# Optimization experiments

Hardware: AMD Instinct MI355X
Metric: run time of the kernel (lower is better)

The kernel has to match this reference:

```python
import jax, jax.numpy as jnp
import numpy as np
import math

T_LEN, BATCH, DIN, DH, DT = 512, 64, 512, 512, 128


def _u(key, shape, std):
    return jax.random.uniform(key, shape, jnp.float32, -std, std)


def setup_inputs() -> dict:
    key = jax.random.key(0)
    ks = jax.random.split(key, 32)
    std = 1.0 / math.sqrt(DH)
    inp = {
        'x': jax.random.normal(ks[0], (T_LEN, BATCH, DIN), jnp.float32),
        'topic': jax.random.normal(ks[1], (BATCH, DT), jnp.float32),
        'mask': jnp.ones((T_LEN, BATCH), jnp.float32),
        # weights stored as [in, out] (transpose of nn.Linear), uniform(-std, std)
        'W_x2zr': _u(ks[2], (DIN, 2 * DH), std),
        'W_tp2zr_x': _u(ks[3], (DT, 2 * DH), std),
        'W_xtp2z': _u(ks[4], (DH, DH), std),
        'b_xtp2z': _u(ks[5], (DH,), std),
        'W_xtp2r': _u(ks[6], (DH, DH), std),
        'b_xtp2r': _u(ks[7], (DH,), std),
        'W_h2zr': _u(ks[8], (DH, 2 * DH), std),
        'W_tp2zr_h': _u(ks[9], (DT, 2 * DH), std),
        'W_htp2z': _u(ks[10], (DH, DH), std),
        'W_htp2r': _u(ks[11], (DH, DH), std),
        'W_x2h': _u(ks[12], (DIN, DH), std),
        'W_tp2h_x': _u(ks[13], (DT, DH), std),
        'W_xtp2h': _u(ks[14], (DH, DH), std),
        'b_xtp2h': _u(ks[15], (DH,), std),
        'W_h2h': _u(ks[16], (DH, DH), std),
        'W_tp2h_h': _u(ks[17], (DT, DH), std),
        'W_htp2h': _u(ks[18], (DH, DH), std),
    }
    return inp


def _tpgru_forward(x, topic, mask,
                   W_x2zr, W_tp2zr_x, W_xtp2z, b_xtp2z, W_xtp2r, b_xtp2r,
                   W_h2zr, W_tp2zr_h, W_htp2z, W_htp2r,
                   W_x2h, W_tp2h_x, W_xtp2h, b_xtp2h,
                   W_h2h, W_tp2h_h, W_htp2h):
    # Precompute all time-parallel (input-side) projections outside the scan.
    ZR_x = x @ W_x2zr                          # [T,B,2H]
    tp_zr_x = topic @ W_tp2zr_x                # [B,2H]
    tp_zr_h = topic @ W_tp2zr_h                # [B,2H]
    Z_xtp, R_xtp = jnp.split(ZR_x * tp_zr_x[None], 2, axis=-1)
    ZR_xtp = jnp.concatenate([Z_xtp @ W_xtp2z + b_xtp2z,
                              R_xtp @ W_xtp2r + b_xtp2r], axis=-1)  # [T,B,2H]
    tp_h_x = topic @ W_tp2h_x                  # [B,H]
    tp_h_h = topic @ W_tp2h_h                  # [B,H]
    H_xtp = ((x @ W_x2h) * tp_h_x[None]) @ W_xtp2h + b_xtp2h        # [T,B,H]

    def step(h_, inputs):
        zr_xtp, h_xtp, m = inputs              # [B,2H], [B,H], [B]
        zr_htp = (h_ @ W_h2zr) * tp_zr_h
        z_htp, r_htp = jnp.split(zr_htp, 2, axis=-1)
        pre_zr = jax.nn.sigmoid(zr_xtp + jnp.concatenate(
            [z_htp @ W_htp2z, r_htp @ W_htp2r], axis=-1))
        z, r = jnp.split(pre_zr, 2, axis=-1)
        h = jnp.tanh(h_xtp + r * (((h_ @ W_h2h) * tp_h_h) @ W_htp2h))
        h = (1.0 - z) * h + z * h_
        m = m[:, None]
        h = m * h + (1.0 - m) * h_
        return h, h

    h0 = jnp.zeros((x.shape[1], W_h2h.shape[0]), x.dtype)
    hT, output = jax.lax.scan(step, h0, (ZR_xtp, H_xtp, mask))
    return output, hT[None]                    # [T,B,H], [1,B,H]


def reference(x, topic, mask,
              W_x2zr, W_tp2zr_x, W_xtp2z, b_xtp2z, W_xtp2r, b_xtp2r,
              W_h2zr, W_tp2zr_h, W_htp2z, W_htp2r,
              W_x2h, W_tp2h_x, W_xtp2h, b_xtp2h,
              W_h2h, W_tp2h_h, W_htp2h):
    return _tpgru_forward(x, topic, mask,
                          W_x2zr, W_tp2zr_x, W_xtp2z, b_xtp2z, W_xtp2r, b_xtp2r,
                          W_h2zr, W_tp2zr_h, W_htp2z, W_htp2r,
                          W_x2h, W_tp2h_x, W_xtp2h, b_xtp2h,
                          W_h2h, W_tp2h_h, W_htp2h)
```

## Files before the change

### kernel.cpp

```cpp
#include <hip/hip_runtime.h>
#include <stdint.h>
#include <stddef.h>


#define T_LEN 512
#define BATCH 64
#define DIN   512
#define DH    512
#define DT    128

typedef __attribute__((ext_vector_type(8))) short short8;
typedef __attribute__((ext_vector_type(4))) float f32x4;

static __device__ __forceinline__ float bf2f(unsigned short u) {
  unsigned v = ((unsigned)u) << 16;
  return __builtin_bit_cast(float, v);
}
static __device__ __forceinline__ unsigned short f2bf(float f) {
  unsigned v = __builtin_bit_cast(unsigned, f);
  unsigned r = (v + 0x7fffu + ((v >> 16) & 1u)) >> 16;
  return (unsigned short)r;
}
static __device__ __forceinline__ float sigmoid_f(float x) {
  return 1.f / (1.f + __expf(-x));
}
static __device__ __forceinline__ float tanh_f(float x) {
  float e = __expf(-2.f * fabsf(x));
  float t = (1.f - e) / (1.f + e);
  return copysignf(t, x);
}

__global__ __launch_bounds__(256) void k_cvt(const float* __restrict__ src,
                                             unsigned short* __restrict__ dst,
                                             int n8) {
  for (int idx = blockIdx.x * 256 + threadIdx.x; idx < n8; idx += gridDim.x * 256) {
    const float4* s = (const float4*)src + 2 * (size_t)idx;
    float4 a = s[0], b = s[1];
    unsigned short d[8];
    d[0] = f2bf(a.x); d[1] = f2bf(a.y); d[2] = f2bf(a.z); d[3] = f2bf(a.w);
    d[4] = f2bf(b.x); d[5] = f2bf(b.y); d[6] = f2bf(b.z); d[7] = f2bf(b.w);
    *(uint4*)(dst + (size_t)idx * 8) = *(const uint4*)d;
  }
}

__global__ __launch_bounds__(256) void k_tr(const float* __restrict__ src,
                                            unsigned short* __restrict__ dst,
                                            int K, int N) {
  __shared__ float t[32][33];
  const int tx = threadIdx.x & 31, ty = threadIdx.x >> 5;
  const int k0 = blockIdx.y * 32, n0 = blockIdx.x * 32;
  for (int i = ty; i < 32; i += 8)
    t[i][tx] = src[(size_t)(k0 + i) * N + n0 + tx];
  __syncthreads();
  for (int i = ty; i < 32; i += 8)
    dst[(size_t)(n0 + i) * K + k0 + tx] = f2bf(t[tx][i]);
}

__global__ __launch_bounds__(256) void k_topic(
    const float* __restrict__ topic,
    const float* __restrict__ Wzx,
    const float* __restrict__ Wzh,
    const float* __restrict__ Whx,
    const float* __restrict__ Whh,
    float* __restrict__ tzx, float* __restrict__ tzh,
    float* __restrict__ thx, float* __restrict__ thh)
{
  const int b = blockIdx.x;
  __shared__ float tp[DT];
  if (threadIdx.x < DT) tp[threadIdx.x] = topic[b * DT + threadIdx.x];
  __syncthreads();
  for (int c = threadIdx.x; c < 3072; c += 256) {
    const float* wp; float* op; int ld, cc;
    if (c < 1024)      { wp = Wzx; ld = 1024; cc = c;        op = &tzx[b*1024 + cc]; }
    else if (c < 2048) { wp = Wzh; ld = 1024; cc = c - 1024; op = &tzh[b*1024 + cc]; }
    else if (c < 2560) { wp = Whx; ld = 512;  cc = c - 2048; op = &thx[b*512  + cc]; }
    else               { wp = Whh; ld = 512;  cc = c - 2560; op = &thh[b*512  + cc]; }
    float acc = 0.f;
    #pragma unroll 4
    for (int k = 0; k < DT; ++k) acc += tp[k] * wp[(size_t)k * ld + cc];
    *op = acc;
  }
}

template<int EPI>
__global__ __launch_bounds__(256) void gemm128(
    const unsigned short* __restrict__ A, int lda,
    const unsigned short* __restrict__ BT, int ldb,
    const float* __restrict__ rs, int ldrs,
    const float* __restrict__ bias,
    unsigned short* __restrict__ C, int ldc, int K)
{
  __shared__ unsigned short As[128][48];
  __shared__ unsigned short Bs[128][48];
  const int tid = threadIdx.x;
  const int n0 = blockIdx.x * 128;
  const int m0 = blockIdx.y * 128;
  const int wv = tid >> 6, lane = tid & 63;
  const int lh = lane & 15, quad = lane >> 4, q8 = quad * 8;
  const int wr = wv >> 1, wc = wv & 1;
  const int srow = tid >> 1, scol = (tid & 1) * 16;

  f32x4 acc[4][4] = {};

  for (int k0 = 0; k0 < K; k0 += 32) {
    uint4 a4[2], b4[2];
    {
      const unsigned short* ap = A  + (size_t)(m0 + srow) * lda + k0 + scol;
      const unsigned short* bp = BT + (size_t)(n0 + srow) * ldb + k0 + scol;
      a4[0] = ((const uint4*)ap)[0]; a4[1] = ((const uint4*)ap)[1];
      b4[0] = ((const uint4*)bp)[0]; b4[1] = ((const uint4*)bp)[1];
    }
    __syncthreads();
    *(uint4*)(&As[srow][scol])     = a4[0];
    *(uint4*)(&As[srow][scol + 8]) = a4[1];
    *(uint4*)(&Bs[srow][scol])     = b4[0];
    *(uint4*)(&Bs[srow][scol + 8]) = b4[1];
    __syncthreads();
    short8 af[4], bf[4];
    #pragma unroll
    for (int i = 0; i < 4; ++i) {
      af[i] = *(const short8*)(&As[wr * 64 + i * 16 + lh][q8]);
      bf[i] = *(const short8*)(&Bs[wc * 64 + i * 16 + lh][q8]);
    }
    #pragma unroll
    for (int i = 0; i < 4; ++i)
      #pragma unroll
      for (int j = 0; j < 4; ++j)
        acc[i][j] = __builtin_amdgcn_mfma_f32_16x16x32_bf16(af[i], bf[j], acc[i][j], 0, 0, 0);
  }

  #pragma unroll
  for (int i = 0; i < 4; ++i)
    #pragma unroll
    for (int j = 0; j < 4; ++j)
      #pragma unroll
      for (int r = 0; r < 4; ++r) {
        int row = m0 + wr * 64 + i * 16 + quad * 4 + r;
        int col = n0 + wc * 64 + j * 16 + lh;
        float v = acc[i][j][r];
        if (EPI == 0) v *= rs[(size_t)(row & 63) * ldrs + col];
        else          v += bias[col];
        C[(size_t)row * ldc + col] = f2bf(v);
      }
}

__global__ __launch_bounds__(256) void k_comb128(
    const float* __restrict__ W1, int ld1, int off1,
    const unsigned short* __restrict__ W2T,
    const float* __restrict__ S, int ldS, int offS,
    unsigned short* __restrict__ Cout)
{
  __shared__ unsigned short As[128][48];
  __shared__ unsigned short Bs[128][48];
  __shared__ float sS[512];
  const int tid = threadIdx.x;
  const int n0 = blockIdx.x * 128;
  const int m0 = blockIdx.y * 128;
  const int b  = blockIdx.z;
  const int wv = tid >> 6, lane = tid & 63;
  const int lh = lane & 15, quad = lane >> 4, q8 = quad * 8;
  const int wr = wv >> 1, wc = wv & 1;
  const int srow = tid >> 1, scol = (tid & 1) * 16;

  sS[tid]       = S[(size_t)b * ldS + offS + tid];
  sS[tid + 256] = S[(size_t)b * ldS + offS + tid + 256];
  __syncthreads();

  f32x4 acc[4][4] = {};

  for (int k0 = 0; k0 < 512; k0 += 32) {
    unsigned short a8[16]; uint4 b4[2];
    {
      const float* ap = W1 + (size_t)(m0 + srow) * ld1 + off1 + k0 + scol;
      const unsigned short* bp = W2T + (size_t)(n0 + srow) * 512 + k0 + scol;
      b4[0] = ((const uint4*)bp)[0]; b4[1] = ((const uint4*)bp)[1];
      float4 f0 = ((const float4*)ap)[0], f1 = ((const float4*)ap)[1];
      float4 f2 = ((const float4*)ap)[2], f3 = ((const float4*)ap)[3];
      const float* sp = &sS[k0 + scol];
      a8[0]  = f2bf(f0.x * sp[0]);  a8[1]  = f2bf(f0.y * sp[1]);
      a8[2]  = f2bf(f0.z * sp[2]);  a8[3]  = f2bf(f0.w * sp[3]);
      a8[4]  = f2bf(f1.x * sp[4]);  a8[5]  = f2bf(f1.y * sp[5]);
      a8[6]  = f2bf(f1.z * sp[6]);  a8[7]  = f2bf(f1.w * sp[7]);
      a8[8]  = f2bf(f2.x * sp[8]);  a8[9]  = f2bf(f2.y * sp[9]);
      a8[10] = f2bf(f2.z * sp[10]); a8[11] = f2bf(f2.w * sp[11]);
      a8[12] = f2bf(f3.x * sp[12]); a8[13] = f2bf(f3.y * sp[13]);
      a8[14] = f2bf(f3.z * sp[14]); a8[15] = f2bf(f3.w * sp[15]);
    }
    __syncthreads();
    *(uint4*)(&As[srow][scol])     = *(const uint4*)(a8);
    *(uint4*)(&As[srow][scol + 8]) = *(const uint4*)(a8 + 8);
    *(uint4*)(&Bs[srow][scol])     = b4[0];
    *(uint4*)(&Bs[srow][scol + 8]) = b4[1];
    __syncthreads();
    short8 af[4], bf[4];
    #pragma unroll
    for (int i = 0; i < 4; ++i) {
      af[i] = *(const short8*)(&As[wr * 64 + i * 16 + lh][q8]);
      bf[i] = *(const short8*)(&Bs[wc * 64 + i * 16 + lh][q8]);
    }
    #pragma unroll
    for (int i = 0; i < 4; ++i)
      #pragma unroll
      for (int j = 0; j < 4; ++j)
        acc[i][j] = __builtin_amdgcn_mfma_f32_16x16x32_bf16(af[i], bf[j], acc[i][j], 0, 0, 0);
  }

  #pragma unroll
  for (int i = 0; i < 4; ++i)
    #pragma unroll
    for (int j = 0; j < 4; ++j)
      #pragma unroll
      for (int r = 0; r < 4; ++r) {
        int row = m0 + wr * 64 + i * 16 + quad * 4 + r;
        int col = n0 + wc * 64 + j * 16 + lh;
        Cout[(size_t)b * 262144 + (size_t)row * 512 + col] = f2bf(acc[i][j][r]);
      }
}

__global__ __launch_bounds__(512) void k_quant(
    const unsigned short* __restrict__ tmp,
    signed char* __restrict__ q,
    float* __restrict__ sc)
{
  const int b = blockIdx.x;
  const int c = threadIdx.x;
  const unsigned short* tb = tmp + (size_t)b * 262144 + c;
  float m = 0.f;
  #pragma unroll 8
  for (int k = 0; k < 512; ++k) m = fmaxf(m, fabsf(bf2f(tb[(size_t)k * 512])));
  float s = m / 127.f;
  float inv = (m > 0.f) ? 127.f / m : 0.f;
  sc[b * 512 + c] = s;
  signed char* qb = q + (size_t)b * 262144 + c;
  #pragma unroll 8
  for (int k = 0; k < 512; ++k) {
    float v = bf2f(tb[(size_t)k * 512]) * inv;
    int iv = (int)rintf(v);
    iv = iv > 127 ? 127 : (iv < -127 ? -127 : iv);
    qb[(size_t)k * 512] = (signed char)iv;
  }
}

static __device__ __forceinline__ void accum8q(float* a, float hk, uint2 v) {
  union { uint2 u; signed char c[8]; } x; x.u = v;
  #pragma unroll
  for (int e = 0; e < 8; ++e) a[e] += hk * (float)x.c[e];
}

__global__ __launch_bounds__(512) void k_scan3(
    const signed char* __restrict__ Az,
    const signed char* __restrict__ Ar,
    const signed char* __restrict__ Ah,
    const float* __restrict__ scZ,
    const float* __restrict__ scR,
    const float* __restrict__ scH,
    const unsigned short* __restrict__ ZRx,
    const unsigned short* __restrict__ Hx,
    const float* __restrict__ mask,
    unsigned* __restrict__ pub,
    float* out)
{
  const int g = blockIdx.x;
  const int b = g >> 3;
  const int w = g & 7;
  const int c0 = w * 64;
  const int t = threadIdx.x;
  const int chunk = t & 7;
  const int ph = t >> 3;
  __shared__ float hs[512];
  __shared__ float part[24][8][68];
  __shared__ float red[192];

  const size_t mbase = (size_t)b * 262144 + (size_t)ph * 512 + c0 + chunk * 8;
  const signed char* pz0 = Az + mbase;
  const signed char* pr0 = Ar + mbase;
  const signed char* pv0 = Ah + mbase;

  unsigned* pubB0 = pub + (size_t)b * 512;
  unsigned* pubB1 = pub + (size_t)(64 + b) * 512;

  float s_z = 0.f, s_r = 0.f, s_h = 0.f;
  if (t < 64) {
    int gc = c0 + t;
    s_z = scZ[b * 512 + gc];
    s_r = scR[b * 512 + gc];
    s_h = scH[b * 512 + gc];
  }

  float hold = 0.f;
  for (int tm = 0; tm < T_LEN; ++tm) {
    unsigned* pubC = (tm & 1) ? pubB1 : pubB0;
    unsigned* pubP = (tm & 1) ? pubB0 : pubB1;
    const size_t itb = (size_t)tm * BATCH + b;

    float g_zx = 0.f, g_rx = 0.f, g_hx = 0.f, g_m = 0.f;
    if (t < 64) {
      int gc = c0 + t;
      g_zx = bf2f(ZRx[itb * 1024 + gc]);
      g_rx = bf2f(ZRx[itb * 1024 + 512 + gc]);
      g_hx = bf2f(Hx[itb * 512 + gc]);
      g_m  = mask[itb];
    }
    uint2 cz = *(const uint2*)(pz0);
    uint2 cr = *(const uint2*)(pr0);
    uint2 cv = *(const uint2*)(pv0);

    if (t < 8) {
      const unsigned* tagp = pubC + t * 64 + 32;
      while ((int)__hip_atomic_load(tagp, __ATOMIC_RELAXED, __HIP_MEMORY_SCOPE_AGENT) < tm)
        ;
    }
    __syncthreads();
    if (t < 256) {
      unsigned v = __hip_atomic_load(pubC + (t >> 5) * 64 + (t & 31),
                                     __ATOMIC_RELAXED, __HIP_MEMORY_SCOPE_AGENT);
      int col = (t >> 5) * 64 + (t & 31) * 2;
      hs[col]     = bf2f((unsigned short)(v & 0xffffu));
      hs[col + 1] = bf2f((unsigned short)(v >> 16));
    }
    __syncthreads();

    float az[8] = {0,0,0,0,0,0,0,0};
    float ar[8] = {0,0,0,0,0,0,0,0};
    float av[8] = {0,0,0,0,0,0,0,0};
    #pragma unroll
    for (int j = 0; j < 8; ++j) {
      uint2 nz, nr, nv;
      if (j < 7) {
        nz = *(const uint2*)(pz0 + (size_t)(j + 1) * 64 * 512);
        nr = *(const uint2*)(pr0 + (size_t)(j + 1) * 64 * 512);
        nv = *(const uint2*)(pv0 + (size_t)(j + 1) * 64 * 512);
      }
      float hk = hs[ph + 64 * j];
      accum8q(az, hk, cz);
      accum8q(ar, hk, cr);
      accum8q(av, hk, cv);
      if (j < 7) { cz = nz; cr = nr; cv = nv; }
    }
    #pragma unroll
    for (int e = 0; e < 8; ++e) {
      part[e][chunk][ph]      = az[e];
      part[8 + e][chunk][ph]  = ar[e];
      part[16 + e][chunk][ph] = av[e];
    }
    __syncthreads();

    if (t < 192) {
      const float* row = &part[t >> 3][t & 7][0];
      float p0 = 0.f, p1 = 0.f, p2 = 0.f, p3 = 0.f;
      #pragma unroll
      for (int q = 0; q < 16; ++q) {
        float4 v = *(const float4*)(row + 4 * q);
        float s = (v.x + v.y) + (v.z + v.w);
        if ((q & 3) == 0) p0 += s;
        else if ((q & 3) == 1) p1 += s;
        else if ((q & 3) == 2) p2 += s;
        else p3 += s;
      }
      int e = t >> 3, ch = t & 7;
      int mat = e >> 3, col = ch * 8 + (e & 7);
      red[mat * 64 + col] = (p0 + p1) + (p2 + p3);
    }
    __syncthreads();

    if (t < 64) {
      float z  = sigmoid_f(red[t] * s_z + g_zx);
      float r  = sigmoid_f(red[64 + t] * s_r + g_rx);
      float hv = tanh_f(g_hx + r * (red[128 + t] * s_h));
      float hnew = (1.f - z) * hv + z * hold;
      hnew = g_m * hnew + (1.f - g_m) * hold;
      hold = hnew;
      int gc = c0 + t;
      out[itb * 512 + gc] = hnew;
      if (tm == T_LEN - 1)
        out[(size_t)T_LEN * BATCH * 512 + (size_t)b * 512 + gc] = hnew;
      int hb = (int)f2bf(hnew);
      unsigned lo = (unsigned)__shfl(hb, 2 * t);
      unsigned hi = (unsigned)__shfl(hb, 2 * t + 1);
      if (t < 32)
        __hip_atomic_store(pubP + w * 64 + t, lo | (hi << 16),
                           __ATOMIC_RELAXED, __HIP_MEMORY_SCOPE_AGENT);
      asm volatile("s_waitcnt vmcnt(0)" ::: "memory");
      if (t == 0)
        __hip_atomic_store(pubP + w * 64 + 32, (unsigned)(tm + 1),
                           __ATOMIC_RELAXED, __HIP_MEMORY_SCOPE_AGENT);
    }
  }
}

extern "C" void kernel_launch(void* const* d_in, const int* in_sizes, int n_in,
                              void* d_out, int out_size, void* d_ws, size_t ws_size,
                              hipStream_t stream) {
  (void)in_sizes; (void)n_in; (void)out_size; (void)ws_size;
  const float* x        = (const float*)d_in[0];
  const float* topic    = (const float*)d_in[1];
  const float* mask     = (const float*)d_in[2];
  const float* W_x2zr   = (const float*)d_in[3];
  const float* W_tp2zrx = (const float*)d_in[4];
  const float* W_xtp2z  = (const float*)d_in[5];
  const float* b_xtp2z  = (const float*)d_in[6];
  const float* W_xtp2r  = (const float*)d_in[7];
  const float* b_xtp2r  = (const float*)d_in[8];
  const float* W_h2zr   = (const float*)d_in[9];
  const float* W_tp2zrh = (const float*)d_in[10];
  const float* W_htp2z  = (const float*)d_in[11];
  const float* W_htp2r  = (const float*)d_in[12];
  const float* W_x2h    = (const float*)d_in[13];
  const float* W_tp2hx  = (const float*)d_in[14];
  const float* W_xtp2h  = (const float*)d_in[15];
  const float* b_xtp2h  = (const float*)d_in[16];
  const float* W_h2h    = (const float*)d_in[17];
  const float* W_tp2hh  = (const float*)d_in[18];
  const float* W_htp2h  = (const float*)d_in[19];
  float* out = (float*)d_out;

  char* w = (char*)d_ws;
  unsigned* pub = (unsigned*)w;      w += (size_t)2 * 64 * 8 * 64 * 4;
  float* tzx = (float*)w;           w += (size_t)BATCH * 1024 * 4;
  float* tzh = (float*)w;           w += (size_t)BATCH * 1024 * 4;
  float* thx = (float*)w;           w += (size_t)BATCH * 512 * 4;
  float* thh = (float*)w;           w += (size_t)BATCH * 512 * 4;
  unsigned short* ZRxtp = (unsigned short*)w; w += (size_t)T_LEN * BATCH * 1024 * 2;
  unsigned short* Hxtp  = (unsigned short*)w; w += (size_t)T_LEN * BATCH * 512 * 2;
  unsigned short* SCR   = (unsigned short*)w; w += (size_t)T_LEN * BATCH * 1024 * 2;
  unsigned short* AhM   = (unsigned short*)w; w += (size_t)BATCH * 512 * 512 * 2;
  unsigned short* WzrT  = (unsigned short*)w; w += (size_t)1024 * 512 * 2;
  unsigned short* WzT   = (unsigned short*)w; w += (size_t)512 * 512 * 2;
  unsigned short* WrT   = (unsigned short*)w; w += (size_t)512 * 512 * 2;
  unsigned short* WxhT  = (unsigned short*)w; w += (size_t)512 * 512 * 2;
  unsigned short* WhpT  = (unsigned short*)w; w += (size_t)512 * 512 * 2;
  unsigned short* W2zT  = (unsigned short*)w; w += (size_t)512 * 512 * 2;
  unsigned short* W2rT  = (unsigned short*)w; w += (size_t)512 * 512 * 2;
  unsigned short* W2hT  = (unsigned short*)w; w += (size_t)512 * 512 * 2;
  float* scZ = (float*)w;           w += (size_t)BATCH * 512 * 4;
  float* scR = (float*)w;           w += (size_t)BATCH * 512 * 4;
  float* scH = (float*)w;           w += (size_t)BATCH * 512 * 4;
  unsigned short* ZRs = SCR;
  unsigned short* Xhs = SCR;
  unsigned short* xb  = AhM;
  unsigned short* tmpA = SCR;
  signed char* Aq  = (signed char*)SCR + (size_t)32 * 1024 * 1024;
  signed char* AqZ = Aq;
  signed char* AqR = Aq + (size_t)BATCH * 512 * 512;
  signed char* AqH = Aq + (size_t)2 * BATCH * 512 * 512;

  const int M = T_LEN * BATCH;

  hipMemsetAsync(pub, 0, (size_t)2 * 64 * 8 * 64 * 4, stream);

  k_cvt<<<2048, 256, 0, stream>>>(x, xb, (int)((size_t)M * DIN / 8));
  k_tr<<<dim3(1024/32, 512/32), 256, 0, stream>>>(W_x2zr,  WzrT, 512, 1024);
  k_tr<<<dim3( 512/32, 512/32), 256, 0, stream>>>(W_xtp2z, WzT,  512,  512);
  k_tr<<<dim3( 512/32, 512/32), 256, 0, stream>>>(W_xtp2r, WrT,  512,  512);
  k_tr<<<dim3( 512/32, 512/32), 256, 0, stream>>>(W_x2h,   WxhT, 512,  512);
  k_tr<<<dim3( 512/32, 512/32), 256, 0, stream>>>(W_xtp2h, WhpT, 512,  512);
  k_tr<<<dim3( 512/32, 512/32), 256, 0, stream>>>(W_htp2z, W2zT, 512,  512);
  k_tr<<<dim3( 512/32, 512/32), 256, 0, stream>>>(W_htp2r, W2rT, 512,  512);
  k_tr<<<dim3( 512/32, 512/32), 256, 0, stream>>>(W_htp2h, W2hT, 512,  512);

  k_topic<<<BATCH, 256, 0, stream>>>(topic, W_tp2zrx, W_tp2zrh, W_tp2hx, W_tp2hh,
                                     tzx, tzh, thx, thh);
  gemm128<0><<<dim3(1024/128, M/128), 256, 0, stream>>>(
      xb, DIN, WzrT, 512, tzx, 1024, nullptr, ZRs, 1024, DIN);
  gemm128<1><<<dim3(512/128, M/128), 256, 0, stream>>>(
      ZRs, 1024, WzT, 512, nullptr, 0, b_xtp2z, ZRxtp, 1024, 512);
  gemm128<1><<<dim3(512/128, M/128), 256, 0, stream>>>(
      ZRs + 512, 1024, WrT, 512, nullptr, 0, b_xtp2r, ZRxtp + 512, 1024, 512);
  gemm128<0><<<dim3(512/128, M/128), 256, 0, stream>>>(
      xb, DIN, WxhT, 512, thx, 512, nullptr, Xhs, 512, DIN);
  gemm128<1><<<dim3(512/128, M/128), 256, 0, stream>>>(
      Xhs, 512, WhpT, 512, nullptr, 0, b_xtp2h, Hxtp, 512, 512);

  k_comb128<<<dim3(4, 4, 64), 256, 0, stream>>>(W_h2zr, 1024,   0, W2zT, tzh, 1024,   0, tmpA);
  k_quant<<<64, 512, 0, stream>>>(tmpA, AqZ, scZ);
  k_comb128<<<dim3(4, 4, 64), 256, 0, stream>>>(W_h2zr, 1024, 512, W2rT, tzh, 1024, 512, tmpA);
  k_quant<<<64, 512, 0, stream>>>(tmpA, AqR, scR);
  k_comb128<<<dim3(4, 4, 64), 256, 0, stream>>>(W_h2h,   512,   0, W2hT, thh,  512,   0, tmpA);
  k_quant<<<64, 512, 0, stream>>>(tmpA, AqH, scH);

  k_scan3<<<512, 512, 0, stream>>>(AqZ, AqR, AqH, scZ, scR, scH,
                                   ZRxtp, Hxtp, mask, pub, out);
}
```

Measured before the change: 4.540 ms.

## Split quantization into parallel colmax/quant passes and remove scan barriers

The quantization kernel is split into two kernels that work over 8 row-slices per batch, with an atomicMax reduction of bit-cast absolute values, so 512 blocks run instead of 64. In the recurrent scan, each wave now polls its own publish tag and fills its own 64-wide slice of the hidden state, which removes two block-wide __syncthreads per timestep. Each thread's k-slice becomes 8 contiguous rows, so it reads the hidden values it needs with two float4 loads from its own wave's slice. The global output stores are moved after the publish so the next step's dependency is released sooner. The risk is correctness of the wave-local handoff through shared memory without a barrier, which relies on wave-level ordering of LDS writes and reads.

```diff
diff --git a/kernel.cpp b/kernel.cpp
--- a/kernel.cpp
+++ b/kernel.cpp
@@ -217,23 +217,35 @@
       }
 }
 
-__global__ __launch_bounds__(512) void k_quant(
+__global__ __launch_bounds__(512) void k_colmax(
     const unsigned short* __restrict__ tmp,
+    unsigned* __restrict__ mx)
+{
+  const int b = blockIdx.x, s = blockIdx.y, c = threadIdx.x;
+  const unsigned short* tb = tmp + (size_t)b * 262144 + (size_t)s * 64 * 512 + c;
+  unsigned m = 0;
+  #pragma unroll 8
+  for (int k = 0; k < 64; ++k) {
+    unsigned v = (((unsigned)tb[(size_t)k * 512]) << 16) & 0x7fffffffu;
+    m = m > v ? m : v;
+  }
+  atomicMax(&mx[b * 512 + c], m);
+}
+
+__global__ __launch_bounds__(512) void k_q8(
+    const unsigned short* __restrict__ tmp,
+    const unsigned* __restrict__ mx,
     signed char* __restrict__ q,
     float* __restrict__ sc)
 {
-  const int b = blockIdx.x;
-  const int c = threadIdx.x;
-  const unsigned short* tb = tmp + (size_t)b * 262144 + c;
-  float m = 0.f;
+  const int b = blockIdx.x, s = blockIdx.y, c = threadIdx.x;
+  float m = __builtin_bit_cast(float, mx[b * 512 + c]);
+  float inv = (m > 0.f) ? 127.f / m : 0.f;
+  if (s == 0) sc[b * 512 + c] = m / 127.f;
+  const unsigned short* tb = tmp + (size_t)b * 262144 + (size_t)s * 64 * 512 + c;
+  signed char* qb = q + (size_t)b * 262144 + (size_t)s * 64 * 512 + c;
   #pragma unroll 8
-  for (int k = 0; k < 512; ++k) m = fmaxf(m, fabsf(bf2f(tb[(size_t)k * 512])));
-  float s = m / 127.f;
-  float inv = (m > 0.f) ? 127.f / m : 0.f;
-  sc[b * 512 + c] = s;
-  signed char* qb = q + (size_t)b * 262144 + c;
-  #pragma unroll 8
-  for (int k = 0; k < 512; ++k) {
+  for (int k = 0; k < 64; ++k) {
     float v = bf2f(tb[(size_t)k * 512]) * inv;
     int iv = (int)rintf(v);
     iv = iv > 127 ? 127 : (iv < -127 ? -127 : iv);
@@ -247,7 +259,7 @@
   for (int e = 0; e < 8; ++e) a[e] += hk * (float)x.c[e];
 }
 
-__global__ __launch_bounds__(512) void k_scan3(
+__global__ __launch_bounds__(512) void k_scan4(
     const signed char* __restrict__ Az,
     const signed char* __restrict__ Ar,
     const signed char* __restrict__ Ah,
@@ -267,14 +279,15 @@
   const int t = threadIdx.x;
   const int chunk = t & 7;
   const int ph = t >> 3;
+  const int wv = t >> 6, lane = t & 63;
   __shared__ float hs[512];
   __shared__ float part[24][8][68];
   __shared__ float red[192];
 
-  const size_t mbase = (size_t)b * 262144 + (size_t)ph * 512 + c0 + chunk * 8;
-  const signed char* pz0 = Az + mbase;
-  const signed char* pr0 = Ar + mbase;
-  const signed char* pv0 = Ah + mbase;
+  const size_t abase = (size_t)b * 262144 + (size_t)(8 * ph) * 512 + c0 + chunk * 8;
+  const signed char* pz0 = Az + abase;
+  const signed char* pr0 = Ar + abase;
+  const signed char* pv0 = Ah + abase;
 
   unsigned* pubB0 = pub + (size_t)b * 512;
   unsigned* pubB1 = pub + (size_t)(64 + b) * 512;
@@ -305,37 +318,40 @@
     uint2 cr = *(const uint2*)(pr0);
     uint2 cv = *(const uint2*)(pv0);
 
-    if (t < 8) {
-      const unsigned* tagp = pubC + t * 64 + 32;
+    {
+      const unsigned* tagp = pubC + wv * 64 + 32;
       while ((int)__hip_atomic_load(tagp, __ATOMIC_RELAXED, __HIP_MEMORY_SCOPE_AGENT) < tm)
         ;
-    }
-    __syncthreads();
-    if (t < 256) {
-      unsigned v = __hip_atomic_load(pubC + (t >> 5) * 64 + (t & 31),
+      asm volatile("" ::: "memory");
+    }
+    if (lane < 32) {
+      unsigned v = __hip_atomic_load(pubC + wv * 64 + lane,
                                      __ATOMIC_RELAXED, __HIP_MEMORY_SCOPE_AGENT);
-      int col = (t >> 5) * 64 + (t & 31) * 2;
-      hs[col]     = bf2f((unsigned short)(v & 0xffffu));
-      hs[col + 1] = bf2f((unsigned short)(v >> 16));
-    }
-    __syncthreads();
+      float2 hv;
+      hv.x = bf2f((unsigned short)(v & 0xffffu));
+      hv.y = bf2f((unsigned short)(v >> 16));
+      *(float2*)(&hs[wv * 64 + 2 * lane]) = hv;
+    }
+
+    float4 h0 = *(const float4*)(&hs[8 * ph]);
+    float4 h1 = *(const float4*)(&hs[8 * ph + 4]);
+    float hkv[8] = {h0.x, h0.y, h0.z, h0.w, h1.x, h1.y, h1.z, h1.w};
 
     float az[8] = {0,0,0,0,0,0,0,0};
     float ar[8] = {0,0,0,0,0,0,0,0};
     float av[8] = {0,0,0,0,0,0,0,0};
     #pragma unroll
-    for (int j = 0; j < 8; ++j) {
+    for (int i = 0; i < 8; ++i) {
       uint2 nz, nr, nv;
-      if (j < 7) {
-        nz = *(const uint2*)(pz0 + (size_t)(j + 1) * 64 * 512);
-        nr = *(const uint2*)(pr0 + (size_t)(j + 1) * 64 * 512);
-        nv = *(const uint2*)(pv0 + (size_t)(j + 1) * 64 * 512);
+      if (i < 7) {
+        nz = *(const uint2*)(pz0 + (size_t)(i + 1) * 512);
+        nr = *(const uint2*)(pr0 + (size_t)(i + 1) * 512);
+        nv = *(const uint2*)(pv0 + (size_t)(i + 1) * 512);
       }
-      float hk = hs[ph + 64 * j];
-      accum8q(az, hk, cz);
-      accum8q(ar, hk, cr);
-      accum8q(av, hk, cv);
-      if (j < 7) { cz = nz; cr = nr; cv = nv; }
+      accum8q(az, hkv[i], cz);
+      accum8q(ar, hkv[i], cr);
+      accum8q(av, hkv[i], cv);
+      if (i < 7) { cz = nz; cr = nr; cv = nv; }
     }
     #pragma unroll
     for (int e = 0; e < 8; ++e) {
@@ -371,9 +387,6 @@
       hnew = g_m * hnew + (1.f - g_m) * hold;
       hold = hnew;
       int gc = c0 + t;
-      out[itb * 512 + gc] = hnew;
-      if (tm == T_LEN - 1)
-        out[(size_t)T_LEN * BATCH * 512 + (size_t)b * 512 + gc] = hnew;
       int hb = (int)f2bf(hnew);
       unsigned lo = (unsigned)__shfl(hb, 2 * t);
       unsigned hi = (unsigned)__shfl(hb, 2 * t + 1);
@@ -384,6 +397,9 @@
       if (t == 0)
         __hip_atomic_store(pubP + w * 64 + 32, (unsigned)(tm + 1),
                            __ATOMIC_RELAXED, __HIP_MEMORY_SCOPE_AGENT);
+      out[itb * 512 + gc] = hnew;
+      if (tm == T_LEN - 1)
+        out[(size_t)T_LEN * BATCH * 512 + (size_t)b * 512 + gc] = hnew;
     }
   }
 }
@@ -416,6 +432,9 @@
 
   char* w = (char*)d_ws;
   unsigned* pub = (unsigned*)w;      w += (size_t)2 * 64 * 8 * 64 * 4;
+  unsigned* mxZ = (unsigned*)w;     w += (size_t)BATCH * 512 * 4;
+  unsigned* mxR = (unsigned*)w;     w += (size_t)BATCH * 512 * 4;
+  unsigned* mxH = (unsigned*)w;     w += (size_t)BATCH * 512 * 4;
   float* tzx = (float*)w;           w += (size_t)BATCH * 1024 * 4;
   float* tzh = (float*)w;           w += (size_t)BATCH * 1024 * 4;
   float* thx = (float*)w;           w += (size_t)BATCH * 512 * 4;
@@ -446,7 +465,8 @@
 
   const int M = T_LEN * BATCH;
 
-  hipMemsetAsync(pub, 0, (size_t)2 * 64 * 8 * 64 * 4, stream);
+  hipMemsetAsync(pub, 0, (size_t)2 * 64 * 8 * 64 * 4 + (size_t)3 * BATCH * 512 * 4,
+                 stream);
 
   k_cvt<<<2048, 256, 0, stream>>>(x, xb, (int)((size_t)M * DIN / 8));
   k_tr<<<dim3(1024/32, 512/32), 256, 0, stream>>>(W_x2zr,  WzrT, 512, 1024);
@@ -472,12 +492,15 @@
       Xhs, 512, WhpT, 512, nullptr, 0, b_xtp2h, Hxtp, 512, 512);
 
   k_comb128<<<dim3(4, 4, 64), 256, 0, stream>>>(W_h2zr, 1024,   0, W2zT, tzh, 1024,   0, tmpA);
-  k_quant<<<64, 512, 0, stream>>>(tmpA, AqZ, scZ);
+  k_colmax<<<dim3(64, 8), 512, 0, stream>>>(tmpA, mxZ);
+  k_q8<<<dim3(64, 8), 512, 0, stream>>>(tmpA, mxZ, AqZ, scZ);
   k_comb128<<<dim3(4, 4, 64), 256, 0, stream>>>(W_h2zr, 1024, 512, W2rT, tzh, 1024, 512, tmpA);
-  k_quant<<<64, 512, 0, stream>>>(tmpA, AqR, scR);
+  k_colmax<<<dim3(64, 8), 512, 0, stream>>>(tmpA, mxR);
+  k_q8<<<dim3(64, 8), 512, 0, stream>>>(tmpA, mxR, AqR, scR);
   k_comb128<<<dim3(4, 4, 64), 256, 0, stream>>>(W_h2h,   512,   0, W2hT, thh,  512,   0, tmpA);
-  k_quant<<<64, 512, 0, stream>>>(tmpA, AqH, scH);
-
-  k_scan3<<<512, 512, 0, stream>>>(AqZ, AqR, AqH, scZ, scR, scH,
+  k_colmax<<<dim3(64, 8), 512, 0, stream>>>(tmpA, mxH);
+  k_q8<<<dim3(64, 8), 512, 0, stream>>>(tmpA, mxH, AqH, scH);
+
+  k_scan4<<<512, 512, 0, stream>>>(AqZ, AqR, AqH, scZ, scR, scH,
                                    ZRxtp, Hxtp, mask, pub, out);
 }
```

New measurement: 7.269 ms. +60.1%, slower.
